# Optimization experiments

Hardware: AMD Instinct MI355X
Metric: run time of the kernel (lower is better)

## Reference

```python
import jax, jax.numpy as jnp
import numpy as np

T, N, E, IN_DIM, H = 20, 50000, 800000, 16, 128
NPF = 7  # num_physical_features
EPS = 1e-5


def setup_inputs() -> dict:
    key = jax.random.key(0)
    ks = jax.random.split(key, 24)
    s = 0.05
    inp = {
        'x': jax.random.normal(ks[0], (T, N, IN_DIM), jnp.float32),
        'edge_index': jax.random.randint(ks[1], (2, E), 0, N, jnp.int64),
        # SAGEConv layer 1 (PyG: lin_l on aggregated neighbors w/ bias, lin_r on root no bias)
        'sage1_wl': jax.random.normal(ks[2], (IN_DIM, H), jnp.float32) * s,
        'sage1_bl': jnp.zeros((H,), jnp.float32),
        'sage1_wr': jax.random.normal(ks[3], (IN_DIM, H), jnp.float32) * s,
        # SAGEConv layer 2
        'sage2_wl': jax.random.normal(ks[4], (H, H), jnp.float32) * s,
        'sage2_bl': jnp.zeros((H,), jnp.float32),
        'sage2_wr': jax.random.normal(ks[5], (H, H), jnp.float32) * s,
        # LayerNorm
        'ln_g': jnp.ones((H,), jnp.float32),
        'ln_b': jnp.zeros((H,), jnp.float32),
        # GRU (torch layout: [3H, H], gate order r,z,n)
        'gru_wih': jax.random.normal(ks[6], (3 * H, H), jnp.float32) * s,
        'gru_whh': jax.random.normal(ks[7], (3 * H, H), jnp.float32) * s,
        'gru_bih': jnp.zeros((3 * H,), jnp.float32),
        'gru_bhh': jnp.zeros((3 * H,), jnp.float32),
        # Thickness decoder
        'th_w1': jax.random.normal(ks[8], (H, H), jnp.float32) * s,
        'th_b1': jnp.zeros((H,), jnp.float32),
        'th_w2': jax.random.normal(ks[9], (H, 1), jnp.float32) * s,
        'th_b2': jnp.zeros((1,), jnp.float32),
        # Physical feature decoder
        'ph_w1': jax.random.normal(ks[10], (H, H), jnp.float32) * s,
        'ph_b1': jnp.zeros((H,), jnp.float32),
        'ph_w2': jax.random.normal(ks[11], (H, NPF), jnp.float32) * s,
        'ph_b2': jnp.zeros((NPF,), jnp.float32),
    }
    return inp


def _sage(h, src, dst, deg_inv, wl, bl, wr):
    # mean-aggregate neighbor features over incoming edges, then two linears
    agg = jax.ops.segment_sum(h[src], dst, num_segments=N) * deg_inv[:, None]
    return agg @ wl + bl + h @ wr


def _forward(x, edge_index,
             sage1_wl, sage1_bl, sage1_wr,
             sage2_wl, sage2_bl, sage2_wr,
             ln_g, ln_b,
             gru_wih, gru_whh, gru_bih, gru_bhh,
             th_w1, th_b1, th_w2, th_b2,
             ph_w1, ph_b1, ph_w2, ph_b2):
    src, dst = edge_index[0], edge_index[1]
    deg = jax.ops.segment_sum(jnp.ones((E,), jnp.float32), dst, num_segments=N)
    deg_inv = 1.0 / jnp.maximum(deg, 1.0)

    def encode(xt):  # [N, IN_DIM] -> [N, H]
        h = jax.nn.relu(_sage(xt, src, dst, deg_inv, sage1_wl, sage1_bl, sage1_wr))
        h = jax.nn.relu(_sage(h, src, dst, deg_inv, sage2_wl, sage2_bl, sage2_wr))
        mu = jnp.mean(h, axis=-1, keepdims=True)
        var = jnp.mean(jnp.square(h - mu), axis=-1, keepdims=True)
        return (h - mu) * jax.lax.rsqrt(var + EPS) * ln_g + ln_b

    encoded = jax.lax.map(encode, x)  # [T, N, H]

    # GRU over time, batch = nodes
    def gru_step(h, x_t):
        gi = x_t @ gru_wih.T + gru_bih  # [N, 3H]
        gh = h @ gru_whh.T + gru_bhh
        i_r, i_z, i_n = jnp.split(gi, 3, axis=-1)
        h_r, h_z, h_n = jnp.split(gh, 3, axis=-1)
        r = jax.nn.sigmoid(i_r + h_r)
        z = jax.nn.sigmoid(i_z + h_z)
        n = jnp.tanh(i_n + r * h_n)
        h_new = (1.0 - z) * n + z * h
        return h_new, h_new

    h0 = jnp.zeros((N, H), jnp.float32)
    _, h_temporal = jax.lax.scan(gru_step, h0, encoded)  # [T, N, H]

    th = jax.nn.relu(h_temporal @ th_w1 + th_b1) @ th_w2 + th_b2   # [T, N, 1]
    ph = jax.nn.relu(h_temporal @ ph_w1 + ph_b1) @ ph_w2 + ph_b2   # [T, N, NPF]
    return th, ph


def reference(x, edge_index,
              sage1_wl, sage1_bl, sage1_wr,
              sage2_wl, sage2_bl, sage2_wr,
              ln_g, ln_b,
              gru_wih, gru_whh, gru_bih, gru_bhh,
              th_w1, th_b1, th_w2, th_b2,
              ph_w1, ph_b1, ph_w2, ph_b2):
    return _forward(x, edge_index,
                    sage1_wl, sage1_bl, sage1_wr,
                    sage2_wl, sage2_bl, sage2_wr,
                    ln_g, ln_b,
                    gru_wih, gru_whh, gru_bih, gru_bhh,
                    th_w1, th_b1, th_w2, th_b2,
                    ph_w1, ph_b1, ph_w2, ph_b2)
```

## Files before the change

kernel.cpp:

```cpp
#include <hip/hip_runtime.h>
#include <hip/hip_bf16.h>

#define TT 20
#define NN 50000
#define EE 800000
#define IND 16
#define HH 128
#define NPF 7
#define CC 4
#define NB ((NN + 255) / 256)

typedef __attribute__((ext_vector_type(8))) short bf16x8;
typedef __attribute__((ext_vector_type(4))) float f32x4;
#define MFMA(a, b, c) __builtin_amdgcn_mfma_f32_16x16x32_bf16(a, b, c, 0, 0, 0)

__device__ __forceinline__ unsigned short f2bf(float f) {
    union { float f; unsigned u; } v; v.f = f;
    unsigned r = v.u + 0x7fffu + ((v.u >> 16) & 1u);
    return (unsigned short)(r >> 16);
}
__device__ __forceinline__ float bf2f(unsigned short u) {
    union { unsigned u; float f; } v; v.u = ((unsigned)u) << 16;
    return v.f;
}

__global__ void detect_kernel(const int* ei, int* flag, int E) {
    __shared__ int nz;
    if (threadIdx.x == 0) nz = 0;
    __syncthreads();
    for (int i = threadIdx.x; i < 1024 && i < E; i += blockDim.x)
        if (ei[2 * i + 1] != 0) atomicOr(&nz, 1);
    __syncthreads();
    if (threadIdx.x == 0) *flag = (nz == 0) ? 1 : 0;
}
__device__ __forceinline__ int edge_src(const int* ei, int e, int E, int f) {
    return f ? ei[2 * e] : ei[e];
}
__device__ __forceinline__ int edge_dst(const int* ei, int e, int E, int f) {
    return f ? ei[2 * (E + e)] : ei[E + e];
}
__global__ void count_deg_kernel(const int* ei, const int* flag, int* deg, int E) {
    int e = blockIdx.x * blockDim.x + threadIdx.x;
    if (e >= E) return;
    int f = *flag;
    atomicAdd(&deg[edge_dst(ei, e, E, f)], 1);
}

__global__ __launch_bounds__(256) void sum_blocks_kernel(const int* deg, int* bsum) {
    int i = blockIdx.x * 256 + threadIdx.x;
    int v = (i < NN) ? deg[i] : 0;
#pragma unroll
    for (int o = 1; o <= 32; o <<= 1) v += __shfl_xor(v, o);
    __shared__ int ws[4];
    if ((threadIdx.x & 63) == 0) ws[threadIdx.x >> 6] = v;
    __syncthreads();
    if (threadIdx.x == 0) bsum[blockIdx.x] = ws[0] + ws[1] + ws[2] + ws[3];
}
__global__ __launch_bounds__(256) void scan_blocks_kernel(const int* bsum, int* bbase) {
    __shared__ int arr[256];
    int t = threadIdx.x;
    int v = (t < NB) ? bsum[t] : 0;
    arr[t] = v;
    __syncthreads();
    for (int off = 1; off < 256; off <<= 1) {
        int u = (t >= off) ? arr[t - off] : 0;
        __syncthreads();
        arr[t] += u;
        __syncthreads();
    }
    if (t < NB) bbase[t] = arr[t] - v;
}
__global__ __launch_bounds__(256) void offs_kernel(const int* deg, const int* bbase,
                                                   int* offs, int* cursor,
                                                   float* dinv, int E) {
    __shared__ int arr[256];
    int t = threadIdx.x;
    int i = blockIdx.x * 256 + t;
    int d = (i < NN) ? deg[i] : 0;
    arr[t] = d;
    __syncthreads();
    for (int off = 1; off < 256; off <<= 1) {
        int u = (t >= off) ? arr[t - off] : 0;
        __syncthreads();
        arr[t] += u;
        __syncthreads();
    }
    if (i < NN) {
        int o = bbase[blockIdx.x] + arr[t] - d;
        offs[i] = o;
        cursor[i] = o;
        dinv[i] = 1.0f / (float)(d > 1 ? d : 1);
        if (i == NN - 1) offs[NN] = E;
    }
}
__global__ void fill_csr_kernel(const int* ei, const int* flag, int* cursor,
                                int* csr, int E) {
    int e = blockIdx.x * blockDim.x + threadIdx.x;
    if (e >= E) return;
    int f = *flag;
    int s = edge_src(ei, e, E, f);
    int d = edge_dst(ei, e, E, f);
    int p = atomicAdd(&cursor[d], 1);
    csr[p] = s;
}

__global__ void pack_kernel(const float* src, unsigned short* dst, int tiles,
                            int mode) {
    int id = blockIdx.x * blockDim.x + threadIdx.x;
    if (id >= tiles * 4 * 64) return;
    int lane = id & 63, kk = (id >> 6) & 3, tile = id >> 8;
    int n = tile * 16 + (lane & 15);
    int kbase = kk * 32 + (lane >> 4) * 8;
    unsigned short out[8];
#pragma unroll
    for (int i = 0; i < 8; ++i) {
        int k = kbase + i;
        float v = mode ? src[n * HH + k] : src[k * (tiles * 16) + n];
        out[i] = f2bf(v);
    }
    *(uint4*)(dst + (size_t)id * 8) = *(uint4*)out;
}

__global__ __launch_bounds__(128) void sage1_kernel(
    const float* __restrict__ x, const int* __restrict__ offs,
    const int* __restrict__ csr, const float* __restrict__ dinv,
    const float* __restrict__ wl, const float* __restrict__ bl,
    const float* __restrict__ wr, unsigned short* __restrict__ h1c, int t0) {
    const int tid = threadIdx.x;
    const int ci = blockIdx.y;
    const float* xt = x + (size_t)(t0 + ci) * NN * IND;
    const int m0 = blockIdx.x * 8;
    __shared__ __align__(16) float sAgg[8][IND];
    __shared__ float sX[8][IND];
    {
        int r = tid >> 4, node = m0 + r;
        int l16 = tid & 15, sub = l16 >> 2, q = l16 & 3;
        int e1 = offs[node + 1];
        float4 a0 = make_float4(0.f, 0.f, 0.f, 0.f);
        float4 a1 = make_float4(0.f, 0.f, 0.f, 0.f);
        float4 a2 = make_float4(0.f, 0.f, 0.f, 0.f);
        float4 a3 = make_float4(0.f, 0.f, 0.f, 0.f);
        int e = offs[node] + sub;
        for (; e + 12 < e1; e += 16) {
            int s0 = __builtin_nontemporal_load(&csr[e]);
            int s1 = __builtin_nontemporal_load(&csr[e + 4]);
            int s2 = __builtin_nontemporal_load(&csr[e + 8]);
            int s3 = __builtin_nontemporal_load(&csr[e + 12]);
            float4 v0 = *(const float4*)(xt + (size_t)s0 * IND + q * 4);
            float4 v1 = *(const float4*)(xt + (size_t)s1 * IND + q * 4);
            float4 v2 = *(const float4*)(xt + (size_t)s2 * IND + q * 4);
            float4 v3 = *(const float4*)(xt + (size_t)s3 * IND + q * 4);
            a0.x += v0.x; a0.y += v0.y; a0.z += v0.z; a0.w += v0.w;
            a1.x += v1.x; a1.y += v1.y; a1.z += v1.z; a1.w += v1.w;
            a2.x += v2.x; a2.y += v2.y; a2.z += v2.z; a2.w += v2.w;
            a3.x += v3.x; a3.y += v3.y; a3.z += v3.z; a3.w += v3.w;
        }
        for (; e < e1; e += 4) {
            int s0 = __builtin_nontemporal_load(&csr[e]);
            float4 v0 = *(const float4*)(xt + (size_t)s0 * IND + q * 4);
            a0.x += v0.x; a0.y += v0.y; a0.z += v0.z; a0.w += v0.w;
        }
        float4 acc;
        acc.x = a0.x + a1.x + a2.x + a3.x;
        acc.y = a0.y + a1.y + a2.y + a3.y;
        acc.z = a0.z + a1.z + a2.z + a3.z;
        acc.w = a0.w + a1.w + a2.w + a3.w;
#pragma unroll
        for (int o = 4; o <= 8; o <<= 1) {
            acc.x += __shfl_xor(acc.x, o);
            acc.y += __shfl_xor(acc.y, o);
            acc.z += __shfl_xor(acc.z, o);
            acc.w += __shfl_xor(acc.w, o);
        }
        if (sub == 0) {
            float di = dinv[node];
            acc.x *= di; acc.y *= di; acc.z *= di; acc.w *= di;
            *(float4*)&sAgg[r][q * 4] = acc;
        }
        sX[r][l16] = xt[(size_t)node * IND + l16];
    }
    __syncthreads();
    const int col = tid;
    float acc[8];
    float b = bl[col];
#pragma unroll
    for (int m = 0; m < 8; ++m) acc[m] = b;
#pragma unroll
    for (int k = 0; k < IND; ++k) {
        float wlv = wl[k * HH + col];
        float wrv = wr[k * HH + col];
#pragma unroll
        for (int m = 0; m < 8; ++m) acc[m] += sAgg[m][k] * wlv + sX[m][k] * wrv;
    }
#pragma unroll
    for (int m = 0; m < 8; ++m)
        h1c[((size_t)(m0 + m) * CC + ci) * HH + col] = f2bf(fmaxf(acc[m], 0.f));
}

#define ADD8(acc, v) do {                                     \
    union { unsigned u; float f; } t_;                        \
    t_.u = (v).x << 16;         acc[0] += t_.f;               \
    t_.u = (v).x & 0xffff0000u; acc[1] += t_.f;               \
    t_.u = (v).y << 16;         acc[2] += t_.f;               \
    t_.u = (v).y & 0xffff0000u; acc[3] += t_.f;               \
    t_.u = (v).z << 16;         acc[4] += t_.f;               \
    t_.u = (v).z & 0xffff0000u; acc[5] += t_.f;               \
    t_.u = (v).w << 16;         acc[6] += t_.f;               \
    t_.u = (v).w & 0xffff0000u; acc[7] += t_.f;               \
} while (0)

__global__ __launch_bounds__(256) void sage2_agg_kernel(
    const unsigned short* __restrict__ h1c, const int* __restrict__ offs,
    const int* __restrict__ csr, const float* __restrict__ dinv,
    unsigned short* __restrict__ agg2c) {
    const int wid = threadIdx.x >> 6, lane = threadIdx.x & 63;
    const int n = blockIdx.x * 4 + wid;
    const char* __restrict__ tb = (const char*)h1c;
    const int lb = lane * 16;
    const int e0 = offs[n], e1 = offs[n + 1];
    float A[8][8];
#pragma unroll
    for (int u = 0; u < 8; ++u)
#pragma unroll
        for (int j = 0; j < 8; ++j) A[u][j] = 0.f;
    int e = e0;
    for (; e + 7 < e1; e += 8) {
        int s[8];
#pragma unroll
        for (int u = 0; u < 8; ++u) s[u] = csr[e + u];
        uint4 v[8];
#pragma unroll
        for (int u = 0; u < 8; ++u)
            v[u] = *(const uint4*)(tb + (size_t)s[u] * 1024 + lb);
#pragma unroll
        for (int u = 0; u < 8; ++u) ADD8(A[u], v[u]);
    }
    for (; e < e1; ++e) {
        int s0 = csr[e];
        uint4 v0 = *(const uint4*)(tb + (size_t)s0 * 1024 + lb);
        ADD8(A[0], v0);
    }
    float di = dinv[n];
    unsigned short o[8];
#pragma unroll
    for (int j = 0; j < 8; ++j) {
        float s = ((A[0][j] + A[1][j]) + (A[2][j] + A[3][j])) +
                  ((A[4][j] + A[5][j]) + (A[6][j] + A[7][j]));
        o[j] = f2bf(s * di);
    }
    *(uint4*)((char*)agg2c + (size_t)n * 1024 + lb) = *(uint4*)o;
}

#define LDA(buf, kk)                                                          \
    (*(const bf16x8*)((const char*)(buf) +                                    \
        (((lane & 15) * 256 + (kk) * 64 + (lane >> 4) * 16) ^                 \
         (((lane & 15) & 7) << 4))))

__global__ __launch_bounds__(64) void gru_fused_kernel(
    const unsigned short* __restrict__ agg2c, const unsigned short* __restrict__ h1c,
    const unsigned short* __restrict__ pS2L, const unsigned short* __restrict__ pS2R,
    const float* __restrict__ s2bl, const float* __restrict__ lng,
    const float* __restrict__ lnb,
    const unsigned short* __restrict__ pGI, const unsigned short* __restrict__ pGH,
    const float* __restrict__ bih, const float* __restrict__ bhh,
    float* __restrict__ h, unsigned short* __restrict__ hallc, int ci) {
    const int lane = threadIdx.x;
    const int r0 = blockIdx.x * 16;
    __shared__ unsigned short bufA[16 * 128];
    __shared__ unsigned short bufB[16 * 128];
    __shared__ unsigned short bufH[16 * 128];

#pragma unroll
    for (int j = 0; j < 4; ++j) {
        int off = (lane + 64 * j) * 16;
        int row = off >> 8, colb = off & 255;
        int swz = off ^ ((row & 7) << 4);
        size_t src = (size_t)(r0 + row) * 1024 + (size_t)ci * 256 + colb;
        *(uint4*)((char*)bufA + swz) = *(const uint4*)((const char*)agg2c + src);
        *(uint4*)((char*)bufB + swz) = *(const uint4*)((const char*)h1c + src);
        const float* hs = h + (size_t)r0 * HH + (size_t)(off / 2);
        unsigned short tmp[8];
#pragma unroll
        for (int i = 0; i < 8; ++i) tmp[i] = f2bf(hs[i]);
        *(uint4*)((char*)bufH + swz) = *(uint4*)tmp;
    }
    __syncthreads();

    bf16x8 ae[4], ah[4];
#pragma unroll
    for (int kk = 0; kk < 4; ++kk) { ae[kk] = LDA(bufA, kk); ah[kk] = LDA(bufB, kk); }
    float vE[8][4];
    float sS[4] = {0, 0, 0, 0}, sQ[4] = {0, 0, 0, 0};
#pragma unroll
    for (int c = 0; c < 8; ++c) {
        f32x4 al = {0, 0, 0, 0}, ar = {0, 0, 0, 0};
#pragma unroll
        for (int kk = 0; kk < 4; ++kk) {
            bf16x8 bl = *(const bf16x8*)(pS2L + ((size_t)(c * 4 + kk) * 64 + lane) * 8);
            bf16x8 br = *(const bf16x8*)(pS2R + ((size_t)(c * 4 + kk) * 64 + lane) * 8);
            al = MFMA(ae[kk], bl, al);
            ar = MFMA(ah[kk], br, ar);
        }
        int col = c * 16 + (lane & 15);
        float bb = s2bl[col];
#pragma unroll
        for (int j = 0; j < 4; ++j) {
            float v = fmaxf(al[j] + ar[j] + bb, 0.f);
            vE[c][j] = v; sS[j] += v; sQ[j] += v * v;
        }
    }
#pragma unroll
    for (int o = 1; o <= 8; o <<= 1) {
#pragma unroll
        for (int j = 0; j < 4; ++j) {
            sS[j] += __shfl_xor(sS[j], o);
            sQ[j] += __shfl_xor(sQ[j], o);
        }
    }
    __syncthreads();
#pragma unroll
    for (int c = 0; c < 8; ++c) {
        int col = c * 16 + (lane & 15);
        float g = lng[col], b = lnb[col];
#pragma unroll
        for (int j = 0; j < 4; ++j) {
            float mu = sS[j] * (1.f / 128.f);
            float var = sQ[j] * (1.f / 128.f) - mu * mu;
            float ve = (vE[c][j] - mu) * rsqrtf(var + 1e-5f) * g + b;
            int row = (lane >> 4) * 4 + j;
            int off = ((row * 128 + col) * 2) ^ ((row & 7) << 4);
            *(unsigned short*)((char*)bufA + off) = f2bf(ve);
        }
    }
    __syncthreads();

    bf16x8 xe[4], xh[4];
#pragma unroll
    for (int kk = 0; kk < 4; ++kk) { xe[kk] = LDA(bufA, kk); xh[kk] = LDA(bufH, kk); }
#pragma unroll
    for (int c = 0; c < 8; ++c) {
        f32x4 air = {0,0,0,0}, aiz = {0,0,0,0}, ain = {0,0,0,0};
        f32x4 ahr = {0,0,0,0}, ahz = {0,0,0,0}, ahn = {0,0,0,0};
#pragma unroll
        for (int kk = 0; kk < 4; ++kk) {
            bf16x8 bir = *(const bf16x8*)(pGI + ((size_t)((c     ) * 4 + kk) * 64 + lane) * 8);
            bf16x8 biz = *(const bf16x8*)(pGI + ((size_t)((c +  8) * 4 + kk) * 64 + lane) * 8);
            bf16x8 bin = *(const bf16x8*)(pGI + ((size_t)((c + 16) * 4 + kk) * 64 + lane) * 8);
            bf16x8 bhr = *(const bf16x8*)(pGH + ((size_t)((c     ) * 4 + kk) * 64 + lane) * 8);
            bf16x8 bhz = *(const bf16x8*)(pGH + ((size_t)((c +  8) * 4 + kk) * 64 + lane) * 8);
            bf16x8 bhn = *(const bf16x8*)(pGH + ((size_t)((c + 16) * 4 + kk) * 64 + lane) * 8);
            air = MFMA(xe[kk], bir, air); aiz = MFMA(xe[kk], biz, aiz);
            ain = MFMA(xe[kk], bin, ain);
            ahr = MFMA(xh[kk], bhr, ahr); ahz = MFMA(xh[kk], bhz, ahz);
            ahn = MFMA(xh[kk], bhn, ahn);
        }
        int col = c * 16 + (lane & 15);
        float bir_ = bih[col], biz_ = bih[HH + col], bin_ = bih[2 * HH + col];
        float bhr_ = bhh[col], bhz_ = bhh[HH + col], bhn_ = bhh[2 * HH + col];
#pragma unroll
        for (int j = 0; j < 4; ++j) {
            int row = (lane >> 4) * 4 + j;
            size_t gidx = (size_t)(r0 + row) * HH + col;
            float rr = 1.f / (1.f + expf(-(air[j] + bir_ + ahr[j] + bhr_)));
            float zz = 1.f / (1.f + expf(-(aiz[j] + biz_ + ahz[j] + bhz_)));
            float nn2 = tanhf(ain[j] + bin_ + rr * (ahn[j] + bhn_));
            float hold = h[gidx];
            float hnew = (1.f - zz) * nn2 + zz * hold;
            h[gidx] = hnew;
            hallc[((size_t)(r0 + row) * CC + ci) * HH + col] = f2bf(hnew);
        }
    }
}

__global__ __launch_bounds__(64) void dec_kernel(
    const unsigned short* __restrict__ hall,
    const unsigned short* __restrict__ pT1, const unsigned short* __restrict__ pP1,
    const float* __restrict__ tb1, const float* __restrict__ tw2,
    const float* __restrict__ tb2, const float* __restrict__ pb1,
    const float* __restrict__ pw2, const float* __restrict__ pb2,
    float* __restrict__ out_th, float* __restrict__ out_ph, int t0) {
    const int lane = threadIdx.x;
    const int rc = blockIdx.x * 16;
    const int ci = rc / NN;
    const int n0 = rc - ci * NN;
    const int tg = t0 + ci;
    __shared__ unsigned short bufB[16 * 128];
#pragma unroll
    for (int j = 0; j < 4; ++j) {
        int off = (lane + 64 * j) * 16;
        int row = off >> 8, colb = off & 255;
        int swz = off ^ ((row & 7) << 4);
        *(uint4*)((char*)bufB + swz) =
            *(const uint4*)((const char*)hall +
                            (size_t)(n0 + row) * 1024 + (size_t)ci * 256 + colb);
    }
    __syncthreads();
    bf16x8 xd[4];
#pragma unroll
    for (int kk = 0; kk < 4; ++kk) xd[kk] = LDA(bufB, kk);
    float pt[4] = {0, 0, 0, 0};
    float pf[NPF][4];
#pragma unroll
    for (int f = 0; f < NPF; ++f)
#pragma unroll
        for (int j = 0; j < 4; ++j) pf[f][j] = 0.f;
#pragma unroll
    for (int c = 0; c < 8; ++c) {
        f32x4 at = {0, 0, 0, 0}, ap = {0, 0, 0, 0};
#pragma unroll
        for (int kk = 0; kk < 4; ++kk) {
            bf16x8 bt = *(const bf16x8*)(pT1 + ((size_t)(c * 4 + kk) * 64 + lane) * 8);
            bf16x8 bp = *(const bf16x8*)(pP1 + ((size_t)(c * 4 + kk) * 64 + lane) * 8);
            at = MFMA(xd[kk], bt, at);
            ap = MFMA(xd[kk], bp, ap);
        }
        int col = c * 16 + (lane & 15);
        float b1 = tb1[col], b2 = pb1[col], w2 = tw2[col];
        float wp[NPF];
#pragma unroll
        for (int f = 0; f < NPF; ++f) wp[f] = pw2[col * NPF + f];
#pragma unroll
        for (int j = 0; j < 4; ++j) {
            float a = fmaxf(at[j] + b1, 0.f);
            pt[j] += a * w2;
            float p = fmaxf(ap[j] + b2, 0.f);
#pragma unroll
            for (int f = 0; f < NPF; ++f) pf[f][j] += p * wp[f];
        }
    }
#pragma unroll
    for (int o = 1; o <= 8; o <<= 1) {
#pragma unroll
        for (int j = 0; j < 4; ++j) {
            pt[j] += __shfl_xor(pt[j], o);
#pragma unroll
            for (int f = 0; f < NPF; ++f) pf[f][j] += __shfl_xor(pf[f][j], o);
        }
    }
    if ((lane & 15) == 0) {
        int g = lane >> 4;
#pragma unroll
        for (int j = 0; j < 4; ++j) {
            int gr = n0 + g * 4 + j;
            out_th[(size_t)tg * NN + gr] = pt[j] + tb2[0];
#pragma unroll
            for (int f = 0; f < NPF; ++f)
                out_ph[((size_t)tg * NN + gr) * NPF + f] = pf[f][j] + pb2[f];
        }
    }
}
#undef LDA

extern "C" void kernel_launch(void* const* d_in, const int* in_sizes, int n_in,
                              void* d_out, int out_size, void* d_ws, size_t ws_size,
                              hipStream_t stream) {
    const float* x     = (const float*)d_in[0];
    const int*   ei    = (const int*)d_in[1];
    const float* s1wl  = (const float*)d_in[2];
    const float* s1bl  = (const float*)d_in[3];
    const float* s1wr  = (const float*)d_in[4];
    const float* s2wl  = (const float*)d_in[5];
    const float* s2bl  = (const float*)d_in[6];
    const float* s2wr  = (const float*)d_in[7];
    const float* lng   = (const float*)d_in[8];
    const float* lnb   = (const float*)d_in[9];
    const float* g_wih = (const float*)d_in[10];
    const float* g_whh = (const float*)d_in[11];
    const float* g_bih = (const float*)d_in[12];
    const float* g_bhh = (const float*)d_in[13];
    const float* tw1   = (const float*)d_in[14];
    const float* tb1   = (const float*)d_in[15];
    const float* tw2   = (const float*)d_in[16];
    const float* tb2   = (const float*)d_in[17];
    const float* pw1   = (const float*)d_in[18];
    const float* pb1   = (const float*)d_in[19];
    const float* pw2   = (const float*)d_in[20];
    const float* pb2   = (const float*)d_in[21];

    char* ws = (char*)d_ws;
    size_t o = 0;
    auto alloc = [&](size_t bytes) {
        size_t r = o;
        o += (bytes + 255) & ~(size_t)255;
        return r;
    };
    int*            flag  = (int*)(ws + alloc(4));
    int*            deg   = (int*)(ws + alloc((size_t)NN * 4));
    int*            offs  = (int*)(ws + alloc((size_t)(NN + 1) * 4));
    int*            curs  = (int*)(ws + alloc((size_t)NN * 4));
    int*            csr   = (int*)(ws + alloc((size_t)EE * 4));
    float*          dinv  = (float*)(ws + alloc((size_t)NN * 4));
    int*            bsum  = (int*)(ws + alloc((size_t)NB * 4));
    int*            bbase = (int*)(ws + alloc((size_t)NB * 4));
    unsigned short* pS2L  = (unsigned short*)(ws + alloc(8 * 4 * 64 * 8 * 2));
    unsigned short* pS2R  = (unsigned short*)(ws + alloc(8 * 4 * 64 * 8 * 2));
    unsigned short* pT1   = (unsigned short*)(ws + alloc(8 * 4 * 64 * 8 * 2));
    unsigned short* pP1   = (unsigned short*)(ws + alloc(8 * 4 * 64 * 8 * 2));
    unsigned short* pGI   = (unsigned short*)(ws + alloc(24 * 4 * 64 * 8 * 2));
    unsigned short* pGH   = (unsigned short*)(ws + alloc(24 * 4 * 64 * 8 * 2));
    float*          hbuf  = (float*)(ws + alloc((size_t)NN * HH * 4));
    unsigned short* h1c   = (unsigned short*)(ws + alloc((size_t)NN * CC * HH * 2));
    unsigned short* agg2c = (unsigned short*)(ws + alloc((size_t)NN * CC * HH * 2));
    unsigned short* hallc = agg2c;

    detect_kernel<<<1, 256, 0, stream>>>(ei, flag, EE);
    hipMemsetAsync(deg, 0, (size_t)NN * 4, stream);
    count_deg_kernel<<<(EE + 255) / 256, 256, 0, stream>>>(ei, flag, deg, EE);
    sum_blocks_kernel<<<NB, 256, 0, stream>>>(deg, bsum);
    scan_blocks_kernel<<<1, 256, 0, stream>>>(bsum, bbase);
    offs_kernel<<<NB, 256, 0, stream>>>(deg, bbase, offs, curs, dinv, EE);
    fill_csr_kernel<<<(EE + 255) / 256, 256, 0, stream>>>(ei, flag, curs, csr, EE);
    pack_kernel<<<(8 * 4 * 64 + 255) / 256, 256, 0, stream>>>(s2wl, pS2L, 8, 0);
    pack_kernel<<<(8 * 4 * 64 + 255) / 256, 256, 0, stream>>>(s2wr, pS2R, 8, 0);
    pack_kernel<<<(8 * 4 * 64 + 255) / 256, 256, 0, stream>>>(tw1, pT1, 8, 0);
    pack_kernel<<<(8 * 4 * 64 + 255) / 256, 256, 0, stream>>>(pw1, pP1, 8, 0);
    pack_kernel<<<(24 * 4 * 64 + 255) / 256, 256, 0, stream>>>(g_wih, pGI, 24, 1);
    pack_kernel<<<(24 * 4 * 64 + 255) / 256, 256, 0, stream>>>(g_whh, pGH, 24, 1);
    hipMemsetAsync(hbuf, 0, (size_t)NN * HH * 4, stream);

    float* out = (float*)d_out;
    for (int t0 = 0; t0 < TT; t0 += CC) {
        dim3 g1(NN / 8, CC);
        sage1_kernel<<<g1, 128, 0, stream>>>(x, offs, csr, dinv, s1wl, s1bl,
                                             s1wr, h1c, t0);
        sage2_agg_kernel<<<NN / 4, 256, 0, stream>>>(h1c, offs, csr, dinv, agg2c);
        for (int ci = 0; ci < CC; ++ci) {
            gru_fused_kernel<<<NN / 16, 64, 0, stream>>>(
                agg2c, h1c, pS2L, pS2R, s2bl, lng, lnb, pGI, pGH,
                g_bih, g_bhh, hbuf, hallc, ci);
        }
        dec_kernel<<<CC * NN / 16, 64, 0, stream>>>(
            hallc, pT1, pP1, tb1, tw2, tb2, pb1, pw2, pb2,
            out, out + (size_t)TT * NN, t0);
    }
}
```

Before: 2.636 ms.

## Merge weight pack launches, shrink aggregation unroll, reuse GRU shared buffer

Six weight-packing launches become one kernel that picks its source and destination from the tile index, which cuts launch overhead. The sage2 aggregation loop now keeps four accumulators with an unroll of four instead of eight by eight, lowering register pressure at the cost of fewer loads in flight per wave. The GRU kernel drops its third shared buffer by reusing bufB for the hidden state once the MFMA operands are in registers. It also adds a minimum-blocks launch bound, both aimed at higher occupancy, at the cost of an extra barrier.

```diff
diff --git a/kernel.cpp b/kernel.cpp
--- a/kernel.cpp
+++ b/kernel.cpp
@@ -104,21 +104,32 @@
     csr[p] = s;
 }
 
-__global__ void pack_kernel(const float* src, unsigned short* dst, int tiles,
-                            int mode) {
+__global__ void pack_all_kernel(
+    const float* s2wl, const float* s2wr, const float* tw1, const float* pw1,
+    const float* wih, const float* whh,
+    unsigned short* pS2L, unsigned short* pS2R, unsigned short* pT1,
+    unsigned short* pP1, unsigned short* pGI, unsigned short* pGH) {
     int id = blockIdx.x * blockDim.x + threadIdx.x;
-    if (id >= tiles * 4 * 64) return;
-    int lane = id & 63, kk = (id >> 6) & 3, tile = id >> 8;
+    if (id >= 80 * 256) return;
+    int gt = id >> 8;
+    int lane = id & 63, kk = (id >> 6) & 3;
+    const float* src; unsigned short* dst; int tile, mode, ncols;
+    if (gt < 8)       { src = s2wl; dst = pS2L; tile = gt;      mode = 0; ncols = 128; }
+    else if (gt < 16) { src = s2wr; dst = pS2R; tile = gt - 8;  mode = 0; ncols = 128; }
+    else if (gt < 24) { src = tw1;  dst = pT1;  tile = gt - 16; mode = 0; ncols = 128; }
+    else if (gt < 32) { src = pw1;  dst = pP1;  tile = gt - 24; mode = 0; ncols = 128; }
+    else if (gt < 56) { src = wih;  dst = pGI;  tile = gt - 32; mode = 1; ncols = 384; }
+    else              { src = whh;  dst = pGH;  tile = gt - 56; mode = 1; ncols = 384; }
     int n = tile * 16 + (lane & 15);
     int kbase = kk * 32 + (lane >> 4) * 8;
     unsigned short out[8];
 #pragma unroll
     for (int i = 0; i < 8; ++i) {
         int k = kbase + i;
-        float v = mode ? src[n * HH + k] : src[k * (tiles * 16) + n];
+        float v = mode ? src[n * HH + k] : src[k * ncols + n];
         out[i] = f2bf(v);
     }
-    *(uint4*)(dst + (size_t)id * 8) = *(uint4*)out;
+    *(uint4*)(dst + ((size_t)tile * 256 + kk * 64 + lane) * 8) = *(uint4*)out;
 }
 
 __global__ __launch_bounds__(128) void sage1_kernel(
@@ -218,36 +229,26 @@
     const char* __restrict__ tb = (const char*)h1c;
     const int lb = lane * 16;
     const int e0 = offs[n], e1 = offs[n + 1];
-    float A[8][8];
-#pragma unroll
-    for (int u = 0; u < 8; ++u)
-#pragma unroll
-        for (int j = 0; j < 8; ++j) A[u][j] = 0.f;
+    float a[8] = {0,0,0,0,0,0,0,0}, b[8] = {0,0,0,0,0,0,0,0};
+    float c_[8] = {0,0,0,0,0,0,0,0}, d[8] = {0,0,0,0,0,0,0,0};
     int e = e0;
-    for (; e + 7 < e1; e += 8) {
-        int s[8];
-#pragma unroll
-        for (int u = 0; u < 8; ++u) s[u] = csr[e + u];
-        uint4 v[8];
-#pragma unroll
-        for (int u = 0; u < 8; ++u)
-            v[u] = *(const uint4*)(tb + (size_t)s[u] * 1024 + lb);
-#pragma unroll
-        for (int u = 0; u < 8; ++u) ADD8(A[u], v[u]);
+    for (; e + 3 < e1; e += 4) {
+        int s0 = csr[e], s1 = csr[e + 1], s2 = csr[e + 2], s3 = csr[e + 3];
+        uint4 v0 = *(const uint4*)(tb + (size_t)s0 * 1024 + lb);
+        uint4 v1 = *(const uint4*)(tb + (size_t)s1 * 1024 + lb);
+        uint4 v2 = *(const uint4*)(tb + (size_t)s2 * 1024 + lb);
+        uint4 v3 = *(const uint4*)(tb + (size_t)s3 * 1024 + lb);
+        ADD8(a, v0); ADD8(b, v1); ADD8(c_, v2); ADD8(d, v3);
     }
     for (; e < e1; ++e) {
         int s0 = csr[e];
         uint4 v0 = *(const uint4*)(tb + (size_t)s0 * 1024 + lb);
-        ADD8(A[0], v0);
+        ADD8(a, v0);
     }
     float di = dinv[n];
     unsigned short o[8];
 #pragma unroll
-    for (int j = 0; j < 8; ++j) {
-        float s = ((A[0][j] + A[1][j]) + (A[2][j] + A[3][j])) +
-                  ((A[4][j] + A[5][j]) + (A[6][j] + A[7][j]));
-        o[j] = f2bf(s * di);
-    }
+    for (int j = 0; j < 8; ++j) o[j] = f2bf((a[j] + b[j] + c_[j] + d[j]) * di);
     *(uint4*)((char*)agg2c + (size_t)n * 1024 + lb) = *(uint4*)o;
 }
 
@@ -256,7 +257,7 @@
         (((lane & 15) * 256 + (kk) * 64 + (lane >> 4) * 16) ^                 \
          (((lane & 15) & 7) << 4))))
 
-__global__ __launch_bounds__(64) void gru_fused_kernel(
+__global__ __launch_bounds__(64, 4) void gru_fused_kernel(
     const unsigned short* __restrict__ agg2c, const unsigned short* __restrict__ h1c,
     const unsigned short* __restrict__ pS2L, const unsigned short* __restrict__ pS2R,
     const float* __restrict__ s2bl, const float* __restrict__ lng,
@@ -268,7 +269,6 @@
     const int r0 = blockIdx.x * 16;
     __shared__ unsigned short bufA[16 * 128];
     __shared__ unsigned short bufB[16 * 128];
-    __shared__ unsigned short bufH[16 * 128];
 
 #pragma unroll
     for (int j = 0; j < 4; ++j) {
@@ -278,17 +278,26 @@
         size_t src = (size_t)(r0 + row) * 1024 + (size_t)ci * 256 + colb;
         *(uint4*)((char*)bufA + swz) = *(const uint4*)((const char*)agg2c + src);
         *(uint4*)((char*)bufB + swz) = *(const uint4*)((const char*)h1c + src);
+    }
+    __syncthreads();
+
+    bf16x8 ae[4], ah[4];
+#pragma unroll
+    for (int kk = 0; kk < 4; ++kk) { ae[kk] = LDA(bufA, kk); ah[kk] = LDA(bufB, kk); }
+    __syncthreads();
+
+#pragma unroll
+    for (int j = 0; j < 4; ++j) {
+        int off = (lane + 64 * j) * 16;
+        int row = off >> 8;
+        int swz = off ^ ((row & 7) << 4);
         const float* hs = h + (size_t)r0 * HH + (size_t)(off / 2);
         unsigned short tmp[8];
 #pragma unroll
         for (int i = 0; i < 8; ++i) tmp[i] = f2bf(hs[i]);
-        *(uint4*)((char*)bufH + swz) = *(uint4*)tmp;
-    }
-    __syncthreads();
-
-    bf16x8 ae[4], ah[4];
-#pragma unroll
-    for (int kk = 0; kk < 4; ++kk) { ae[kk] = LDA(bufA, kk); ah[kk] = LDA(bufB, kk); }
+        *(uint4*)((char*)bufB + swz) = *(uint4*)tmp;
+    }
+
     float vE[8][4];
     float sS[4] = {0, 0, 0, 0}, sQ[4] = {0, 0, 0, 0};
 #pragma unroll
@@ -336,7 +345,7 @@
 
     bf16x8 xe[4], xh[4];
 #pragma unroll
-    for (int kk = 0; kk < 4; ++kk) { xe[kk] = LDA(bufA, kk); xh[kk] = LDA(bufH, kk); }
+    for (int kk = 0; kk < 4; ++kk) { xe[kk] = LDA(bufA, kk); xh[kk] = LDA(bufB, kk); }
 #pragma unroll
     for (int c = 0; c < 8; ++c) {
         f32x4 air = {0,0,0,0}, aiz = {0,0,0,0}, ain = {0,0,0,0};
@@ -510,12 +519,8 @@
     scan_blocks_kernel<<<1, 256, 0, stream>>>(bsum, bbase);
     offs_kernel<<<NB, 256, 0, stream>>>(deg, bbase, offs, curs, dinv, EE);
     fill_csr_kernel<<<(EE + 255) / 256, 256, 0, stream>>>(ei, flag, curs, csr, EE);
-    pack_kernel<<<(8 * 4 * 64 + 255) / 256, 256, 0, stream>>>(s2wl, pS2L, 8, 0);
-    pack_kernel<<<(8 * 4 * 64 + 255) / 256, 256, 0, stream>>>(s2wr, pS2R, 8, 0);
-    pack_kernel<<<(8 * 4 * 64 + 255) / 256, 256, 0, stream>>>(tw1, pT1, 8, 0);
-    pack_kernel<<<(8 * 4 * 64 + 255) / 256, 256, 0, stream>>>(pw1, pP1, 8, 0);
-    pack_kernel<<<(24 * 4 * 64 + 255) / 256, 256, 0, stream>>>(g_wih, pGI, 24, 1);
-    pack_kernel<<<(24 * 4 * 64 + 255) / 256, 256, 0, stream>>>(g_whh, pGH, 24, 1);
+    pack_all_kernel<<<(80 * 256 + 255) / 256, 256, 0, stream>>>(
+        s2wl, s2wr, tw1, pw1, g_wih, g_whh, pS2L, pS2R, pT1, pP1, pGI, pGH);
     hipMemsetAsync(hbuf, 0, (size_t)NN * HH * 4, stream);
 
     float* out = (float*)d_out;
```

After: 2.358 ms. -10.6%, faster.
